# Performance work log

Hardware: AMD Instinct MI355X
Metric: run time of the kernel (lower is better)

Reference implementation:

```python
import jax, jax.numpy as jnp
import numpy as np

IN_CHANNELS = 3
WINDOW_SIZE = 11
SIGMA = 1.5
PAD = WINDOW_SIZE // 2


def _create_window():
    # NOTE: faithful to the original repo, the exponent is POSITIVE (a known
    # bug in AntixK/PyTorch-VAE); we replicate the exact math.
    x = np.arange(WINDOW_SIZE, dtype=np.float64)
    k = np.exp((x - WINDOW_SIZE // 2) ** 2 / (2.0 * SIGMA ** 2))
    k = (k / k.sum()).astype(np.float32)
    w2d = np.outer(k, k)  # [K, K]
    # depthwise kernel, OIHW with groups=C -> [C, 1, K, K]
    return jnp.asarray(np.broadcast_to(w2d, (IN_CHANNELS, 1, WINDOW_SIZE, WINDOW_SIZE)).copy())


def _dwconv(x, w):
    return jax.lax.conv_general_dilated(
        x, w, window_strides=(1, 1), padding=[(PAD, PAD), (PAD, PAD)],
        feature_group_count=IN_CHANNELS,
        dimension_numbers=('NCHW', 'OIHW', 'NCHW'))


def _avg_pool2(x):
    B, C, H, W = x.shape
    return x.reshape(B, C, H // 2, 2, W // 2, 2).mean(axis=(3, 5))


def _ssim(img1, img2, window):
    mu1 = _dwconv(img1, window)
    mu2 = _dwconv(img2, window)
    mu1_sq = mu1 * mu1
    mu2_sq = mu2 * mu2
    mu1_mu2 = mu1 * mu2
    sigma1_sq = _dwconv(img1 * img1, window) - mu1_sq
    sigma2_sq = _dwconv(img2 * img2, window) - mu2_sq
    sigma12 = _dwconv(img1 * img2, window) - mu1_mu2
    C1 = 0.01 ** 2
    C2 = 0.03 ** 2
    v1 = 2.0 * sigma12 + C2
    v2 = sigma1_sq + sigma2_sq + C2
    cs = jnp.mean(v1 / v2)
    ssim_map = (2.0 * mu1_mu2 + C1) * v1 / ((mu1_sq + mu2_sq + C1) * v2)
    return jnp.mean(ssim_map), cs  # size_average=True


def setup_inputs() -> dict:
    key = jax.random.key(0)
    k1, k2 = jax.random.split(key)
    shape = (32, 3, 512, 512)
    img1 = jax.random.uniform(k1, shape, dtype=jnp.float32)
    img2 = jax.random.uniform(k2, shape, dtype=jnp.float32)
    return {"img1": img1, "img2": img2}


def reference(img1, img2):
    weights = jnp.asarray([0.0448, 0.2856, 0.3001, 0.2363, 0.1333], dtype=jnp.float32)
    window = _create_window()
    mssim, mcs = [], []
    for _ in range(5):
        sim, cs = _ssim(img1, img2, window)
        mssim.append(sim)
        mcs.append(cs)
        img1 = _avg_pool2(img1)
        img2 = _avg_pool2(img2)
    mssim = jnp.stack(mssim)
    mcs = jnp.stack(mcs)
    pow1 = mcs ** weights
    pow2 = mssim ** weights
    output = jnp.prod(pow1[:-1] * pow2[-1])
    return 1.0 - output
```

## Files before the change

### kernel.cpp

```cpp
#include <hip/hip_runtime.h>
#include <cmath>

typedef short bf16x8 __attribute__((ext_vector_type(8)));
typedef float f32x4 __attribute__((ext_vector_type(4)));

struct Coeffs { float k[11]; };

__device__ __forceinline__ ushort f2bf(float f) {
    unsigned u = __float_as_uint(f);
    u += 0x7fff + ((u >> 16) & 1);
    return (ushort)(u >> 16);
}

__device__ __forceinline__ unsigned pk2(float lo, float hi) {
    unsigned d;
    asm("v_cvt_pk_bf16_f32 %0, %1, %2" : "=v"(d) : "v"(lo), "v"(hi));
    return d;
}

__device__ __forceinline__ float frcp(float x) { return __builtin_amdgcn_rcpf(x); }

__device__ __forceinline__ float4 ld4s(const float* __restrict__ p, int r, int c, int H, int W) {
    float4 v = make_float4(0.f, 0.f, 0.f, 0.f);
    if (r >= 0 && r < H) {
        const float* row = p + (size_t)r * W;
        if (c >= 0 && c + 3 < W) {
            v = *reinterpret_cast<const float4*>(row + c);
        } else {
            if (c + 0 >= 0 && c + 0 < W) v.x = row[c + 0];
            if (c + 1 >= 0 && c + 1 < W) v.y = row[c + 1];
            if (c + 2 >= 0 && c + 2 < W) v.z = row[c + 2];
            if (c + 3 >= 0 && c + 3 < W) v.w = row[c + 3];
        }
    }
    return v;
}

union FragU { ushort us[8]; bf16x8 v; uint4 q; };
union RdU   { uint4 q; bf16x8 v; };

__global__ __launch_bounds__(64)
void init_frag_kernel(uint4* __restrict__ tab, Coeffs cf) {
    const int lane = threadIdx.x;
    const int lj   = lane & 15;
    const int part = lane >> 4;
    FragU bHf, aVf;
    #pragma unroll
    for (int i = 0; i < 8; ++i) {
        const int kk = part * 8 + i;
        const int tH = kk - lj - 3;
        const int tV = kk - lj;
        float vH = 0.f, vV = 0.f;
        #pragma unroll
        for (int tt = 0; tt < 11; ++tt) {
            vH = (tH == tt) ? cf.k[tt] : vH;
            vV = (tV == tt) ? cf.k[tt] : vV;
        }
        bHf.us[i] = f2bf(vH);
        aVf.us[i] = f2bf(vV);
    }
    tab[lane]      = bHf.q;
    tab[64 + lane] = aVf.q;
}

__global__ __launch_bounds__(256)
void ssim_level_mfma(const float* __restrict__ i1, const float* __restrict__ i2,
                     float* __restrict__ o1, float* __restrict__ o2,
                     int H, int W,
                     double* __restrict__ accum,
                     const uint4* __restrict__ frag_tab)
{
    __shared__ __align__(16) ushort H_T[5][32][64];
    __shared__ double red[2][4];

    const int tid  = threadIdx.x;
    const int lane = tid & 63;
    const int lj   = lane & 15;
    const int part = lane >> 4;
    const int swz  = (lane & 7) << 4;
    const int wv   = __builtin_amdgcn_readfirstlane(tid) >> 6;

    const int bc = blockIdx.z;
    const int r0 = blockIdx.y * 32;
    const int c0 = blockIdx.x * 32;
    const float* p1 = i1 + (size_t)bc * H * W;
    const float* p2 = i2 + (size_t)bc * H * W;

    RdU bHu, aVu;
    bHu.q = frag_tab[lane];
    aVu.q = frag_tab[64 + lane];
    const bf16x8 bH = bHu.v;
    const bf16x8 aV = aVu.v;

    const f32x4 zf = {0.f, 0.f, 0.f, 0.f};

    if (wv < 3) {
        const int gr = r0 - 5 + wv * 16 + lj;
        char* st = (char*)&H_T[0][0][0] + lj * 128 + ((wv * 32 + part * 8) ^ swz);
        #pragma unroll
        for (int cg = 0; cg < 2; ++cg) {
            const int gc = c0 - 8 + cg * 16 + part * 8;
            float a8[8], b8[8];
            if (gr >= 0 && gr < H && gc >= 0 && gc + 8 <= W) {
                const size_t idx = (size_t)gr * W + gc;
                float4 va0 = *reinterpret_cast<const float4*>(p1 + idx);
                float4 va1 = *reinterpret_cast<const float4*>(p1 + idx + 4);
                float4 vb0 = *reinterpret_cast<const float4*>(p2 + idx);
                float4 vb1 = *reinterpret_cast<const float4*>(p2 + idx + 4);
                a8[0]=va0.x; a8[1]=va0.y; a8[2]=va0.z; a8[3]=va0.w;
                a8[4]=va1.x; a8[5]=va1.y; a8[6]=va1.z; a8[7]=va1.w;
                b8[0]=vb0.x; b8[1]=vb0.y; b8[2]=vb0.z; b8[3]=vb0.w;
                b8[4]=vb1.x; b8[5]=vb1.y; b8[6]=vb1.z; b8[7]=vb1.w;
            } else {
                float4 va0 = ld4s(p1, gr, gc, H, W);
                float4 va1 = ld4s(p1, gr, gc + 4, H, W);
                float4 vb0 = ld4s(p2, gr, gc, H, W);
                float4 vb1 = ld4s(p2, gr, gc + 4, H, W);
                a8[0]=va0.x; a8[1]=va0.y; a8[2]=va0.z; a8[3]=va0.w;
                a8[4]=va1.x; a8[5]=va1.y; a8[6]=va1.z; a8[7]=va1.w;
                b8[0]=vb0.x; b8[1]=vb0.y; b8[2]=vb0.z; b8[3]=vb0.w;
                b8[4]=vb1.x; b8[5]=vb1.y; b8[6]=vb1.z; b8[7]=vb1.w;
            }

            unsigned pkf[5][4];
            #pragma unroll
            for (int e = 0; e < 4; ++e) {
                const float a0 = a8[2*e], a1 = a8[2*e+1];
                const float b0 = b8[2*e], b1 = b8[2*e+1];
                pkf[0][e] = pk2(a0, a1);
                pkf[1][e] = pk2(b0, b1);
                pkf[2][e] = pk2(a0*a0, a1*a1);
                pkf[3][e] = pk2(b0*b0, b1*b1);
                pkf[4][e] = pk2(a0*b0, a1*b1);
            }
            #pragma unroll
            for (int s = 0; s < 5; ++s) {
                RdU fr;
                fr.q.x = pkf[s][0]; fr.q.y = pkf[s][1];
                fr.q.z = pkf[s][2]; fr.q.w = pkf[s][3];
                f32x4 d = __builtin_amdgcn_mfma_f32_16x16x32_bf16(fr.v, bH, zf, 0, 0, 0);
                *(uint2*)(st + cg * 2048 + s * 4096)
                    = make_uint2(pk2(d[0], d[1]), pk2(d[2], d[3]));
            }
        }
    } else if (o1 != nullptr) {
        const int p = tid - 192;
        const int i = p & 15;
        const int h = p >> 4;
        const size_t idx = (size_t)(r0 + 2 * i) * W + (c0 + 8 * h);
        const float* pa = p1 + idx;
        const float* pb = p2 + idx;
        float4 a00 = *reinterpret_cast<const float4*>(pa);
        float4 a01 = *reinterpret_cast<const float4*>(pa + 4);
        float4 a10 = *reinterpret_cast<const float4*>(pa + W);
        float4 a11 = *reinterpret_cast<const float4*>(pa + W + 4);
        float4 b00 = *reinterpret_cast<const float4*>(pb);
        float4 b01 = *reinterpret_cast<const float4*>(pb + 4);
        float4 b10 = *reinterpret_cast<const float4*>(pb + W);
        float4 b11 = *reinterpret_cast<const float4*>(pb + W + 4);
        float4 oa, ob;
        oa.x = 0.25f*(a00.x+a00.y+a10.x+a10.y); oa.y = 0.25f*(a00.z+a00.w+a10.z+a10.w);
        oa.z = 0.25f*(a01.x+a01.y+a11.x+a11.y); oa.w = 0.25f*(a01.z+a01.w+a11.z+a11.w);
        ob.x = 0.25f*(b00.x+b00.y+b10.x+b10.y); ob.y = 0.25f*(b00.z+b00.w+b10.z+b10.w);
        ob.z = 0.25f*(b01.x+b01.y+b11.x+b11.y); ob.w = 0.25f*(b01.z+b01.w+b11.z+b11.w);
        const int W2 = W >> 1;
        const size_t base = (size_t)bc * (size_t)(H >> 1) * W2
                          + (size_t)(r0/2 + i) * W2 + (c0/2 + 4*h);
        *reinterpret_cast<float4*>(o1 + base) = oa;
        *reinterpret_cast<float4*>(o2 + base) = ob;
    }
    __syncthreads();

    const int rg2 = wv >> 1;
    const int cg2 = wv & 1;
    const char* hb = (const char*)&H_T[0][0][0] + cg2 * 2048 + lj * 128
                   + ((rg2 * 32 + part * 16) ^ swz);
    f32x4 acc[5];
    #pragma unroll
    for (int s = 0; s < 5; ++s) {
        RdU br;
        br.q = *(const uint4*)(hb + s * 4096);
        acc[s] = __builtin_amdgcn_mfma_f32_16x16x32_bf16(aV, br.v, zf, 0, 0, 0);
    }

    const float C1 = 1e-4f, C2 = 9e-4f;
    float ssim_acc = 0.f, cs_acc = 0.f;
    #pragma unroll
    for (int r = 0; r < 4; ++r) {
        const float mu1 = acc[0][r], mu2 = acc[1][r];
        const float m11 = acc[2][r], m22 = acc[3][r], m12 = acc[4][r];
        const float mu1s = mu1 * mu1, mu2s = mu2 * mu2, mu12 = mu1 * mu2;
        const float v1 = 2.f * (m12 - mu12) + C2;
        const float v2 = (m11 - mu1s) + (m22 - mu2s) + C2;
        const float r2 = frcp(v2);
        const float rd = frcp(mu1s + mu2s + C1);
        cs_acc   += v1 * r2;
        ssim_acc += (2.f * mu12 + C1) * v1 * r2 * rd;
    }

    #pragma unroll
    for (int off = 32; off > 0; off >>= 1) {
        ssim_acc += __shfl_down(ssim_acc, off);
        cs_acc   += __shfl_down(cs_acc, off);
    }
    if (lane == 0) { red[0][wv] = (double)ssim_acc; red[1][wv] = (double)cs_acc; }
    __syncthreads();
    if (tid == 0) {
        double s = red[0][0] + red[0][1] + red[0][2] + red[0][3];
        double c = red[1][0] + red[1][1] + red[1][2] + red[1][3];
        int slot = (blockIdx.x + blockIdx.y * 3 + blockIdx.z * 7) & 63;
        atomicAdd(&accum[slot], s);
        atomicAdd(&accum[64 + slot], c);
    }
}

#define SPF 33
#define HRF 42

__global__ __launch_bounds__(256)
void ssim_level_f32(const float* __restrict__ i1, const float* __restrict__ i2,
                    float* __restrict__ o1, float* __restrict__ o2,
                    int H, int W,
                    double* __restrict__ accum, Coeffs cf)
{
    __shared__ __align__(16) float varr[5][HRF][SPF];
    __shared__ __align__(16) float phl[2][16][16];
    __shared__ double red[2][4];

    const int tid = threadIdx.x;
    const int bc  = blockIdx.z;
    const int r0 = blockIdx.y * 32;
    const int c0 = blockIdx.x * 32;
    const float* p1 = i1 + (size_t)bc * H * W;
    const float* p2 = i2 + (size_t)bc * H * W;

    const int row_rel = tid >> 2;
    const int j  = tid & 3;
    const int cl = 8 * j;
    float hpA[4], hpB[4];
    bool pool_thread = false;

    if (tid < HRF * 4) {
        const int gr  = r0 + row_rel - 5;
        const int gcb = c0 + cl - 8;

        float a[24], b[24];
        if (gr >= 0 && gr < H && gcb >= 0 && gcb + 24 <= W) {
            const size_t idx = (size_t)gr * W + gcb;
            const float* pa = p1 + idx;
            const float* pb = p2 + idx;
            #pragma unroll
            for (int g = 0; g < 6; ++g) {
                float4 va = *reinterpret_cast<const float4*>(pa + 4 * g);
                float4 vb = *reinterpret_cast<const float4*>(pb + 4 * g);
                a[4*g+0]=va.x; a[4*g+1]=va.y; a[4*g+2]=va.z; a[4*g+3]=va.w;
                b[4*g+0]=vb.x; b[4*g+1]=vb.y; b[4*g+2]=vb.z; b[4*g+3]=vb.w;
            }
        } else {
            #pragma unroll
            for (int g = 0; g < 6; ++g) {
                float4 va = ld4s(p1, gr, gcb + 4 * g, H, W);
                float4 vb = ld4s(p2, gr, gcb + 4 * g, H, W);
                a[4*g+0]=va.x; a[4*g+1]=va.y; a[4*g+2]=va.z; a[4*g+3]=va.w;
                b[4*g+0]=vb.x; b[4*g+1]=vb.y; b[4*g+2]=vb.z; b[4*g+3]=vb.w;
            }
        }

        float acc[5][8] = {};
        #pragma unroll
        for (int i = 0; i < 24; ++i) {
            float av = a[i], bv = b[i];
            float pa2 = av * av, pb2 = bv * bv, pab = av * bv;
            #pragma unroll
            for (int jo = 0; jo < 8; ++jo) {
                const int t = i - 3 - jo;
                if (t >= 0 && t <= 10) {
                    const float kk = cf.k[t];
                    acc[0][jo] += kk * av;  acc[1][jo] += kk * bv;
                    acc[2][jo] += kk * pa2; acc[3][jo] += kk * pb2;
                    acc[4][jo] += kk * pab;
                }
            }
        }
        #pragma unroll
        for (int s = 0; s < 5; ++s) {
            *reinterpret_cast<float4*>(&varr[s][row_rel][cl]) =
                make_float4(acc[s][0], acc[s][1], acc[s][2], acc[s][3]);
            *reinterpret_cast<float4*>(&varr[s][row_rel][cl + 4]) =
                make_float4(acc[s][4], acc[s][5], acc[s][6], acc[s][7]);
        }

        if (o1 != nullptr && row_rel >= 5 && row_rel <= 36) {
            #pragma unroll
            for (int p = 0; p < 4; ++p) {
                hpA[p] = a[8 + 2*p] + a[9 + 2*p];
                hpB[p] = b[8 + 2*p] + b[9 + 2*p];
            }
            if (row_rel & 1) {
                const int i = (row_rel - 5) >> 1;
                *reinterpret_cast<float4*>(&phl[0][i][4*j]) = make_float4(hpA[0],hpA[1],hpA[2],hpA[3]);
                *reinterpret_cast<float4*>(&phl[1][i][4*j]) = make_float4(hpB[0],hpB[1],hpB[2],hpB[3]);
            } else if (row_rel >= 6) {
                pool_thread = true;
            }
        }
    }
    __syncthreads();

    if (pool_thread) {
        const int i = (row_rel - 6) >> 1;
        const int W2 = W >> 1;
        float4 qa = *reinterpret_cast<const float4*>(&phl[0][i][4*j]);
        float4 qb = *reinterpret_cast<const float4*>(&phl[1][i][4*j]);
        qa.x = 0.25f*(qa.x + hpA[0]); qa.y = 0.25f*(qa.y + hpA[1]);
        qa.z = 0.25f*(qa.z + hpA[2]); qa.w = 0.25f*(qa.w + hpA[3]);
        qb.x = 0.25f*(qb.x + hpB[0]); qb.y = 0.25f*(qb.y + hpB[1]);
        qb.z = 0.25f*(qb.z + hpB[2]); qb.w = 0.25f*(qb.w + hpB[3]);
        const size_t base = (size_t)bc * (size_t)(H >> 1) * W2
                          + (size_t)(r0/2 + i) * W2 + (c0/2 + 4*j);
        *reinterpret_cast<float4*>(o1 + base) = qa;
        *reinterpret_cast<float4*>(o2 + base) = qb;
    }

    const int col = tid & 31;
    const int rg  = tid >> 5;

    float acc[5][4] = {};
    #pragma unroll
    for (int t = 0; t < 14; ++t) {
        const int m = rg * 4 + t;
        #pragma unroll
        for (int s = 0; s < 5; ++s) {
            const float val = varr[s][m][col];
            #pragma unroll
            for (int i = 0; i < 4; ++i) {
                const int tap = t - i;
                if (tap >= 0 && tap <= 10) acc[s][i] += cf.k[tap] * val;
            }
        }
    }

    const float C1 = 1e-4f, C2 = 9e-4f;
    float ssim_acc = 0.f, cs_acc = 0.f;
    #pragma unroll
    for (int i = 0; i < 4; ++i) {
        const float mu1 = acc[0][i], mu2 = acc[1][i];
        const float m11 = acc[2][i], m22 = acc[3][i], m12 = acc[4][i];
        const float mu1s = mu1 * mu1, mu2s = mu2 * mu2, mu12 = mu1 * mu2;
        const float v1 = 2.f * (m12 - mu12) + C2;
        const float v2 = (m11 - mu1s) + (m22 - mu2s) + C2;
        const float r2 = frcp(v2);
        const float rd = frcp(mu1s + mu2s + C1);
        cs_acc   += v1 * r2;
        ssim_acc += (2.f * mu12 + C1) * v1 * r2 * rd;
    }

    #pragma unroll
    for (int off = 32; off > 0; off >>= 1) {
        ssim_acc += __shfl_down(ssim_acc, off);
        cs_acc   += __shfl_down(cs_acc, off);
    }
    const int wave = tid >> 6, lane = tid & 63;
    if (lane == 0) { red[0][wave] = (double)ssim_acc; red[1][wave] = (double)cs_acc; }
    __syncthreads();
    if (tid == 0) {
        double s = red[0][0] + red[0][1] + red[0][2] + red[0][3];
        double c = red[1][0] + red[1][1] + red[1][2] + red[1][3];
        int slot = (blockIdx.x + blockIdx.y * 3 + blockIdx.z * 7) & 63;
        atomicAdd(&accum[slot], s);
        atomicAdd(&accum[64 + slot], c);
    }
}

__global__ __launch_bounds__(64)
void finalize_kernel(const double* __restrict__ accum,
                     float* __restrict__ out, int BC)
{
    __shared__ double sums[5][2];
    int tid = threadIdx.x;
    for (int lvl = 0; lvl < 5; ++lvl) {
        for (int m = 0; m < 2; ++m) {
            double v = accum[(lvl * 2 + m) * 64 + tid];
            for (int off = 32; off > 0; off >>= 1) v += __shfl_down(v, off);
            if (tid == 0) sums[lvl][m] = v;
        }
    }
    __syncthreads();
    if (tid == 0) {
        const double w[5] = {0.0448, 0.2856, 0.3001, 0.2363, 0.1333};
        double prod = 1.0;
        for (int lvl = 0; lvl < 5; ++lvl) {
            int hw = (512 >> lvl);
            double cnt = (double)BC * (double)hw * (double)hw;
            double mssim = sums[lvl][0] / cnt;
            double mcs   = sums[lvl][1] / cnt;
            if (lvl < 4) {
                prod *= pow(mcs, w[lvl]);
            } else {
                double p2 = pow(mssim, w[4]);
                prod *= p2 * p2 * p2 * p2;
            }
        }
        out[0] = (float)(1.0 - prod);
    }
}

extern "C" void kernel_launch(void* const* d_in, const int* in_sizes, int n_in,
                              void* d_out, int out_size, void* d_ws, size_t ws_size,
                              hipStream_t stream) {
    const float* img1 = (const float*)d_in[0];
    const float* img2 = (const float*)d_in[1];
    float* out = (float*)d_out;
    char* ws = (char*)d_ws;

    const int BC = in_sizes[0] / (512 * 512);

    double* accum = (double*)ws;
    uint4*  ftab  = (uint4*)(ws + 6144);
    size_t off = 8192;
    float* lvl1[5] = {nullptr, nullptr, nullptr, nullptr, nullptr};
    float* lvl2[5] = {nullptr, nullptr, nullptr, nullptr, nullptr};
    for (int l = 1; l < 5; ++l) {
        size_t hw = (size_t)(512 >> l) * (512 >> l);
        lvl1[l] = (float*)(ws + off); off += (size_t)BC * hw * sizeof(float);
        lvl2[l] = (float*)(ws + off); off += (size_t)BC * hw * sizeof(float);
    }

    hipMemsetAsync(accum, 0, 5 * 2 * 64 * sizeof(double), stream);

    Coeffs cf;
    {
        double kd[11], sum = 0.0;
        for (int i = 0; i < 11; ++i) { kd[i] = exp(((double)((i-5)*(i-5))) / 4.5); sum += kd[i]; }
        for (int i = 0; i < 11; ++i) cf.k[i] = (float)(kd[i] / sum);
    }

    init_frag_kernel<<<1, 64, 0, stream>>>(ftab, cf);

    const float* cur1 = img1;
    const float* cur2 = img2;
    for (int lvl = 0; lvl < 5; ++lvl) {
        int H = 512 >> lvl, W = H;
        dim3 grid(W / 32, H / 32, BC);
        float* n1 = (lvl < 4) ? lvl1[lvl + 1] : nullptr;
        float* n2 = (lvl < 4) ? lvl2[lvl + 1] : nullptr;
        if (lvl < 2) {
            ssim_level_mfma<<<grid, 256, 0, stream>>>(cur1, cur2, n1, n2, H, W,
                                                      accum + lvl * 128, ftab);
        } else {
            ssim_level_f32<<<grid, 256, 0, stream>>>(cur1, cur2, n1, n2, H, W,
                                                     accum + lvl * 128, cf);
        }
        cur1 = n1; cur2 = n2;
    }

    finalize_kernel<<<1, 64, 0, stream>>>(accum, out, BC);
}
```

Baseline: 195.0 us.

## Make MFMA SSIM kernel persistent with register double-buffered tile prefetch

Turns the MFMA level kernel into a persistent grid-stride loop over flattened tiles, with the grid capped at 2048 blocks. Global loads for the next tile go into a second register buffer while the current tile is convolved and reduced, so load latency overlaps compute. The downsample wave now reuses the same prefetched registers. The cost is extra registers per thread, which may lower occupancy, plus a fixed grid size that may balance work unevenly.

```diff
diff --git a/kernel.cpp b/kernel.cpp
--- a/kernel.cpp
+++ b/kernel.cpp
@@ -63,70 +63,77 @@
     tab[64 + lane] = aVf.q;
 }
 
-__global__ __launch_bounds__(256)
-void ssim_level_mfma(const float* __restrict__ i1, const float* __restrict__ i2,
-                     float* __restrict__ o1, float* __restrict__ o2,
-                     int H, int W,
-                     double* __restrict__ accum,
-                     const uint4* __restrict__ frag_tab)
+__device__ __forceinline__ void issue_tile_loads(
+    const float* __restrict__ i1, const float* __restrict__ i2,
+    int H, int W, int bc, int r0, int c0,
+    int wv, int lj, int part,
+    float (&SA)[2][8], float (&SB)[2][8])
 {
-    __shared__ __align__(16) ushort H_T[5][32][64];
-    __shared__ double red[2][4];
-
-    const int tid  = threadIdx.x;
-    const int lane = tid & 63;
-    const int lj   = lane & 15;
-    const int part = lane >> 4;
-    const int swz  = (lane & 7) << 4;
-    const int wv   = __builtin_amdgcn_readfirstlane(tid) >> 6;
-
-    const int bc = blockIdx.z;
-    const int r0 = blockIdx.y * 32;
-    const int c0 = blockIdx.x * 32;
     const float* p1 = i1 + (size_t)bc * H * W;
     const float* p2 = i2 + (size_t)bc * H * W;
-
-    RdU bHu, aVu;
-    bHu.q = frag_tab[lane];
-    aVu.q = frag_tab[64 + lane];
-    const bf16x8 bH = bHu.v;
-    const bf16x8 aV = aVu.v;
-
-    const f32x4 zf = {0.f, 0.f, 0.f, 0.f};
-
     if (wv < 3) {
         const int gr = r0 - 5 + wv * 16 + lj;
-        char* st = (char*)&H_T[0][0][0] + lj * 128 + ((wv * 32 + part * 8) ^ swz);
         #pragma unroll
         for (int cg = 0; cg < 2; ++cg) {
             const int gc = c0 - 8 + cg * 16 + part * 8;
-            float a8[8], b8[8];
+            float4 va0, va1, vb0, vb1;
             if (gr >= 0 && gr < H && gc >= 0 && gc + 8 <= W) {
                 const size_t idx = (size_t)gr * W + gc;
-                float4 va0 = *reinterpret_cast<const float4*>(p1 + idx);
-                float4 va1 = *reinterpret_cast<const float4*>(p1 + idx + 4);
-                float4 vb0 = *reinterpret_cast<const float4*>(p2 + idx);
-                float4 vb1 = *reinterpret_cast<const float4*>(p2 + idx + 4);
-                a8[0]=va0.x; a8[1]=va0.y; a8[2]=va0.z; a8[3]=va0.w;
-                a8[4]=va1.x; a8[5]=va1.y; a8[6]=va1.z; a8[7]=va1.w;
-                b8[0]=vb0.x; b8[1]=vb0.y; b8[2]=vb0.z; b8[3]=vb0.w;
-                b8[4]=vb1.x; b8[5]=vb1.y; b8[6]=vb1.z; b8[7]=vb1.w;
+                va0 = *reinterpret_cast<const float4*>(p1 + idx);
+                va1 = *reinterpret_cast<const float4*>(p1 + idx + 4);
+                vb0 = *reinterpret_cast<const float4*>(p2 + idx);
+                vb1 = *reinterpret_cast<const float4*>(p2 + idx + 4);
             } else {
-                float4 va0 = ld4s(p1, gr, gc, H, W);
-                float4 va1 = ld4s(p1, gr, gc + 4, H, W);
-                float4 vb0 = ld4s(p2, gr, gc, H, W);
-                float4 vb1 = ld4s(p2, gr, gc + 4, H, W);
-                a8[0]=va0.x; a8[1]=va0.y; a8[2]=va0.z; a8[3]=va0.w;
-                a8[4]=va1.x; a8[5]=va1.y; a8[6]=va1.z; a8[7]=va1.w;
-                b8[0]=vb0.x; b8[1]=vb0.y; b8[2]=vb0.z; b8[3]=vb0.w;
-                b8[4]=vb1.x; b8[5]=vb1.y; b8[6]=vb1.z; b8[7]=vb1.w;
-            }
-
+                va0 = ld4s(p1, gr, gc, H, W);
+                va1 = ld4s(p1, gr, gc + 4, H, W);
+                vb0 = ld4s(p2, gr, gc, H, W);
+                vb1 = ld4s(p2, gr, gc + 4, H, W);
+            }
+            SA[cg][0]=va0.x; SA[cg][1]=va0.y; SA[cg][2]=va0.z; SA[cg][3]=va0.w;
+            SA[cg][4]=va1.x; SA[cg][5]=va1.y; SA[cg][6]=va1.z; SA[cg][7]=va1.w;
+            SB[cg][0]=vb0.x; SB[cg][1]=vb0.y; SB[cg][2]=vb0.z; SB[cg][3]=vb0.w;
+            SB[cg][4]=vb1.x; SB[cg][5]=vb1.y; SB[cg][6]=vb1.z; SB[cg][7]=vb1.w;
+        }
+    } else {
+        const size_t idx = (size_t)(r0 + 2 * lj) * W + (c0 + part * 8);
+        float4 va0 = *reinterpret_cast<const float4*>(p1 + idx);
+        float4 va1 = *reinterpret_cast<const float4*>(p1 + idx + 4);
+        float4 va2 = *reinterpret_cast<const float4*>(p1 + idx + W);
+        float4 va3 = *reinterpret_cast<const float4*>(p1 + idx + W + 4);
+        float4 vb0 = *reinterpret_cast<const float4*>(p2 + idx);
+        float4 vb1 = *reinterpret_cast<const float4*>(p2 + idx + 4);
+        float4 vb2 = *reinterpret_cast<const float4*>(p2 + idx + W);
+        float4 vb3 = *reinterpret_cast<const float4*>(p2 + idx + W + 4);
+        SA[0][0]=va0.x; SA[0][1]=va0.y; SA[0][2]=va0.z; SA[0][3]=va0.w;
+        SA[0][4]=va1.x; SA[0][5]=va1.y; SA[0][6]=va1.z; SA[0][7]=va1.w;
+        SA[1][0]=va2.x; SA[1][1]=va2.y; SA[1][2]=va2.z; SA[1][3]=va2.w;
+        SA[1][4]=va3.x; SA[1][5]=va3.y; SA[1][6]=va3.z; SA[1][7]=va3.w;
+        SB[0][0]=vb0.x; SB[0][1]=vb0.y; SB[0][2]=vb0.z; SB[0][3]=vb0.w;
+        SB[0][4]=vb1.x; SB[0][5]=vb1.y; SB[0][6]=vb1.z; SB[0][7]=vb1.w;
+        SB[1][0]=vb2.x; SB[1][1]=vb2.y; SB[1][2]=vb2.z; SB[1][3]=vb2.w;
+        SB[1][4]=vb3.x; SB[1][5]=vb3.y; SB[1][6]=vb3.z; SB[1][7]=vb3.w;
+    }
+}
+
+__device__ __forceinline__ void compute_tile(
+    ushort* H_T0, double (*red)[4],
+    const bf16x8 bH, const bf16x8 aV,
+    char* st, const char* hb,
+    int wv, int lane, int tid, int lj, int part,
+    int H, int W, int bc, int r0, int c0, int tile_idx,
+    float (&SA)[2][8], float (&SB)[2][8],
+    float* __restrict__ o1, float* __restrict__ o2,
+    double* __restrict__ accum)
+{
+    const f32x4 zf = {0.f, 0.f, 0.f, 0.f};
+    if (wv < 3) {
+        #pragma unroll
+        for (int cg = 0; cg < 2; ++cg) {
             unsigned pkf[5][4];
             #pragma unroll
             for (int e = 0; e < 4; ++e) {
-                const float a0 = a8[2*e], a1 = a8[2*e+1];
-                const float b0 = b8[2*e], b1 = b8[2*e+1];
+                const float a0 = SA[cg][2*e], a1 = SA[cg][2*e+1];
+                const float b0 = SB[cg][2*e], b1 = SB[cg][2*e+1];
                 pkf[0][e] = pk2(a0, a1);
                 pkf[1][e] = pk2(b0, b1);
                 pkf[2][e] = pk2(a0*a0, a1*a1);
@@ -143,38 +150,24 @@
                     = make_uint2(pk2(d[0], d[1]), pk2(d[2], d[3]));
             }
         }
-    } else if (o1 != nullptr) {
-        const int p = tid - 192;
-        const int i = p & 15;
-        const int h = p >> 4;
-        const size_t idx = (size_t)(r0 + 2 * i) * W + (c0 + 8 * h);
-        const float* pa = p1 + idx;
-        const float* pb = p2 + idx;
-        float4 a00 = *reinterpret_cast<const float4*>(pa);
-        float4 a01 = *reinterpret_cast<const float4*>(pa + 4);
-        float4 a10 = *reinterpret_cast<const float4*>(pa + W);
-        float4 a11 = *reinterpret_cast<const float4*>(pa + W + 4);
-        float4 b00 = *reinterpret_cast<const float4*>(pb);
-        float4 b01 = *reinterpret_cast<const float4*>(pb + 4);
-        float4 b10 = *reinterpret_cast<const float4*>(pb + W);
-        float4 b11 = *reinterpret_cast<const float4*>(pb + W + 4);
+    } else {
         float4 oa, ob;
-        oa.x = 0.25f*(a00.x+a00.y+a10.x+a10.y); oa.y = 0.25f*(a00.z+a00.w+a10.z+a10.w);
-        oa.z = 0.25f*(a01.x+a01.y+a11.x+a11.y); oa.w = 0.25f*(a01.z+a01.w+a11.z+a11.w);
-        ob.x = 0.25f*(b00.x+b00.y+b10.x+b10.y); ob.y = 0.25f*(b00.z+b00.w+b10.z+b10.w);
-        ob.z = 0.25f*(b01.x+b01.y+b11.x+b11.y); ob.w = 0.25f*(b01.z+b01.w+b11.z+b11.w);
+        oa.x = 0.25f*(SA[0][0]+SA[0][1]+SA[1][0]+SA[1][1]);
+        oa.y = 0.25f*(SA[0][2]+SA[0][3]+SA[1][2]+SA[1][3]);
+        oa.z = 0.25f*(SA[0][4]+SA[0][5]+SA[1][4]+SA[1][5]);
+        oa.w = 0.25f*(SA[0][6]+SA[0][7]+SA[1][6]+SA[1][7]);
+        ob.x = 0.25f*(SB[0][0]+SB[0][1]+SB[1][0]+SB[1][1]);
+        ob.y = 0.25f*(SB[0][2]+SB[0][3]+SB[1][2]+SB[1][3]);
+        ob.z = 0.25f*(SB[0][4]+SB[0][5]+SB[1][4]+SB[1][5]);
+        ob.w = 0.25f*(SB[0][6]+SB[0][7]+SB[1][6]+SB[1][7]);
         const int W2 = W >> 1;
         const size_t base = (size_t)bc * (size_t)(H >> 1) * W2
-                          + (size_t)(r0/2 + i) * W2 + (c0/2 + 4*h);
+                          + (size_t)(r0 / 2 + lj) * W2 + (c0 / 2 + part * 4);
         *reinterpret_cast<float4*>(o1 + base) = oa;
         *reinterpret_cast<float4*>(o2 + base) = ob;
     }
     __syncthreads();
 
-    const int rg2 = wv >> 1;
-    const int cg2 = wv & 1;
-    const char* hb = (const char*)&H_T[0][0][0] + cg2 * 2048 + lj * 128
-                   + ((rg2 * 32 + part * 16) ^ swz);
     f32x4 acc[5];
     #pragma unroll
     for (int s = 0; s < 5; ++s) {
@@ -208,9 +201,79 @@
     if (tid == 0) {
         double s = red[0][0] + red[0][1] + red[0][2] + red[0][3];
         double c = red[1][0] + red[1][1] + red[1][2] + red[1][3];
-        int slot = (blockIdx.x + blockIdx.y * 3 + blockIdx.z * 7) & 63;
+        int slot = tile_idx & 63;
         atomicAdd(&accum[slot], s);
         atomicAdd(&accum[64 + slot], c);
+    }
+}
+
+__global__ __launch_bounds__(256)
+void ssim_level_mfma(const float* __restrict__ i1, const float* __restrict__ i2,
+                     float* __restrict__ o1, float* __restrict__ o2,
+                     int H, int W, int logT, int ntiles,
+                     double* __restrict__ accum,
+                     const uint4* __restrict__ frag_tab)
+{
+    __shared__ __align__(16) ushort H_T[5][32][64];
+    __shared__ double red[2][4];
+
+    const int tid  = threadIdx.x;
+    const int lane = tid & 63;
+    const int lj   = lane & 15;
+    const int part = lane >> 4;
+    const int swz  = (lane & 7) << 4;
+    const int wv   = __builtin_amdgcn_readfirstlane(tid) >> 6;
+
+    RdU bHu, aVu;
+    bHu.q = frag_tab[lane];
+    aVu.q = frag_tab[64 + lane];
+    const bf16x8 bH = bHu.v;
+    const bf16x8 aV = aVu.v;
+
+    char* st = (char*)&H_T[0][0][0] + lj * 128 + (((wv < 3 ? wv : 0) * 32 + part * 8) ^ swz);
+    const int rg2 = wv >> 1, cg2 = wv & 1;
+    const char* hb = (const char*)&H_T[0][0][0] + cg2 * 2048 + lj * 128
+                   + ((rg2 * 32 + part * 16) ^ swz);
+
+    const int tmask  = (1 << logT) - 1;
+    const int stride = gridDim.x;
+
+    int idx = blockIdx.x;
+    if (idx >= ntiles) return;
+    int bc = idx >> (2 * logT);
+    int r0 = ((idx >> logT) & tmask) * 32;
+    int c0 = (idx & tmask) * 32;
+
+    float S0A[2][8], S0B[2][8], S1A[2][8], S1B[2][8];
+    issue_tile_loads(i1, i2, H, W, bc, r0, c0, wv, lj, part, S0A, S0B);
+
+    int nbc = 0, nr0 = 0, nc0 = 0;
+    while (true) {
+        int nidx = idx + stride;
+        bool has = nidx < ntiles;
+        if (has) {
+            nbc = nidx >> (2 * logT);
+            nr0 = ((nidx >> logT) & tmask) * 32;
+            nc0 = (nidx & tmask) * 32;
+            issue_tile_loads(i1, i2, H, W, nbc, nr0, nc0, wv, lj, part, S1A, S1B);
+        }
+        compute_tile(&H_T[0][0][0], red, bH, aV, st, hb, wv, lane, tid, lj, part,
+                     H, W, bc, r0, c0, idx, S0A, S0B, o1, o2, accum);
+        if (!has) break;
+        idx = nidx; bc = nbc; r0 = nr0; c0 = nc0;
+
+        nidx = idx + stride;
+        has = nidx < ntiles;
+        if (has) {
+            nbc = nidx >> (2 * logT);
+            nr0 = ((nidx >> logT) & tmask) * 32;
+            nc0 = (nidx & tmask) * 32;
+            issue_tile_loads(i1, i2, H, W, nbc, nr0, nc0, wv, lj, part, S0A, S0B);
+        }
+        compute_tile(&H_T[0][0][0], red, bH, aV, st, hb, wv, lane, tid, lj, part,
+                     H, W, bc, r0, c0, idx, S1A, S1B, o1, o2, accum);
+        if (!has) break;
+        idx = nidx; bc = nbc; r0 = nr0; c0 = nc0;
     }
 }
 
@@ -441,13 +504,18 @@
     const float* cur2 = img2;
     for (int lvl = 0; lvl < 5; ++lvl) {
         int H = 512 >> lvl, W = H;
-        dim3 grid(W / 32, H / 32, BC);
         float* n1 = (lvl < 4) ? lvl1[lvl + 1] : nullptr;
         float* n2 = (lvl < 4) ? lvl2[lvl + 1] : nullptr;
         if (lvl < 2) {
+            int T = W / 32;
+            int logT = (lvl == 0) ? 4 : 3;
+            int ntiles = T * T * BC;
+            int grid = ntiles < 2048 ? ntiles : 2048;
             ssim_level_mfma<<<grid, 256, 0, stream>>>(cur1, cur2, n1, n2, H, W,
+                                                      logT, ntiles,
                                                       accum + lvl * 128, ftab);
         } else {
+            dim3 grid(W / 32, H / 32, BC);
             ssim_level_f32<<<grid, 256, 0, stream>>>(cur1, cur2, n1, n2, H, W,
                                                      accum + lvl * 128, cf);
         }
```

Result: slower. 225.0 us (+15.4%).

## Stage raw input tile in shared memory with cooperative coalesced loads

Applied to the files above, without the earlier changes.

All 256 threads now cooperatively load the 48x48 input halo tile for both images into a shared-memory buffer before any compute. The horizontal MFMA pass and the 2x2 average-pool writer then read from shared memory instead of issuing their own global loads. This removes duplicate global reads between the pooling wave and the conv waves and spreads the loads over all four waves. The cost is an extra barrier, about 20 KB more LDS per block (which may lower occupancy), and possible bank conflicts from the 52-float row pitch.

```diff
diff --git a/kernel.cpp b/kernel.cpp
--- a/kernel.cpp
+++ b/kernel.cpp
@@ -5,6 +5,8 @@
 typedef float f32x4 __attribute__((ext_vector_type(4)));
 
 struct Coeffs { float k[11]; };
+
+#define RPITCH 52
 
 __device__ __forceinline__ ushort f2bf(float f) {
     unsigned u = __float_as_uint(f);
@@ -70,6 +72,7 @@
                      double* __restrict__ accum,
                      const uint4* __restrict__ frag_tab)
 {
+    __shared__ __align__(16) float  RAW[2][48][RPITCH];
     __shared__ __align__(16) ushort H_T[5][32][64];
     __shared__ double red[2][4];
 
@@ -92,35 +95,45 @@
     const bf16x8 bH = bHu.v;
     const bf16x8 aV = aVu.v;
 
+    {
+        const bool interior = (r0 >= 5) && (r0 + 43 <= H) && (c0 >= 8) && (c0 + 40 <= W);
+        #pragma unroll
+        for (int img = 0; img < 2; ++img) {
+            const float* p = img ? p2 : p1;
+            #pragma unroll
+            for (int it = 0; it < 3; ++it) {
+                const int idx = tid + it * 256;
+                if (idx < 576) {
+                    const int row  = idx / 12;
+                    const int colg = idx - row * 12;
+                    const int gr = r0 - 5 + row;
+                    const int gc = c0 - 8 + 4 * colg;
+                    float4 v;
+                    if (interior) {
+                        v = *reinterpret_cast<const float4*>(p + (size_t)gr * W + gc);
+                    } else {
+                        v = ld4s(p, gr, gc, H, W);
+                    }
+                    *reinterpret_cast<float4*>(&RAW[img][row][4 * colg]) = v;
+                }
+            }
+        }
+    }
+    __syncthreads();
+
     const f32x4 zf = {0.f, 0.f, 0.f, 0.f};
-
     if (wv < 3) {
-        const int gr = r0 - 5 + wv * 16 + lj;
+        const int row = wv * 16 + lj;
         char* st = (char*)&H_T[0][0][0] + lj * 128 + ((wv * 32 + part * 8) ^ swz);
         #pragma unroll
         for (int cg = 0; cg < 2; ++cg) {
-            const int gc = c0 - 8 + cg * 16 + part * 8;
-            float a8[8], b8[8];
-            if (gr >= 0 && gr < H && gc >= 0 && gc + 8 <= W) {
-                const size_t idx = (size_t)gr * W + gc;
-                float4 va0 = *reinterpret_cast<const float4*>(p1 + idx);
-                float4 va1 = *reinterpret_cast<const float4*>(p1 + idx + 4);
-                float4 vb0 = *reinterpret_cast<const float4*>(p2 + idx);
-                float4 vb1 = *reinterpret_cast<const float4*>(p2 + idx + 4);
-                a8[0]=va0.x; a8[1]=va0.y; a8[2]=va0.z; a8[3]=va0.w;
-                a8[4]=va1.x; a8[5]=va1.y; a8[6]=va1.z; a8[7]=va1.w;
-                b8[0]=vb0.x; b8[1]=vb0.y; b8[2]=vb0.z; b8[3]=vb0.w;
-                b8[4]=vb1.x; b8[5]=vb1.y; b8[6]=vb1.z; b8[7]=vb1.w;
-            } else {
-                float4 va0 = ld4s(p1, gr, gc, H, W);
-                float4 va1 = ld4s(p1, gr, gc + 4, H, W);
-                float4 vb0 = ld4s(p2, gr, gc, H, W);
-                float4 vb1 = ld4s(p2, gr, gc + 4, H, W);
-                a8[0]=va0.x; a8[1]=va0.y; a8[2]=va0.z; a8[3]=va0.w;
-                a8[4]=va1.x; a8[5]=va1.y; a8[6]=va1.z; a8[7]=va1.w;
-                b8[0]=vb0.x; b8[1]=vb0.y; b8[2]=vb0.z; b8[3]=vb0.w;
-                b8[4]=vb1.x; b8[5]=vb1.y; b8[6]=vb1.z; b8[7]=vb1.w;
-            }
+            const int cb = cg * 16 + part * 8;
+            float4 va0 = *reinterpret_cast<const float4*>(&RAW[0][row][cb]);
+            float4 va1 = *reinterpret_cast<const float4*>(&RAW[0][row][cb + 4]);
+            float4 vb0 = *reinterpret_cast<const float4*>(&RAW[1][row][cb]);
+            float4 vb1 = *reinterpret_cast<const float4*>(&RAW[1][row][cb + 4]);
+            float a8[8] = {va0.x, va0.y, va0.z, va0.w, va1.x, va1.y, va1.z, va1.w};
+            float b8[8] = {vb0.x, vb0.y, vb0.z, vb0.w, vb1.x, vb1.y, vb1.z, vb1.w};
 
             unsigned pkf[5][4];
             #pragma unroll
@@ -144,35 +157,30 @@
             }
         }
     } else if (o1 != nullptr) {
-        const int p = tid - 192;
-        const int i = p & 15;
-        const int h = p >> 4;
-        const size_t idx = (size_t)(r0 + 2 * i) * W + (c0 + 8 * h);
-        const float* pa = p1 + idx;
-        const float* pb = p2 + idx;
-        float4 a00 = *reinterpret_cast<const float4*>(pa);
-        float4 a01 = *reinterpret_cast<const float4*>(pa + 4);
-        float4 a10 = *reinterpret_cast<const float4*>(pa + W);
-        float4 a11 = *reinterpret_cast<const float4*>(pa + W + 4);
-        float4 b00 = *reinterpret_cast<const float4*>(pb);
-        float4 b01 = *reinterpret_cast<const float4*>(pb + 4);
-        float4 b10 = *reinterpret_cast<const float4*>(pb + W);
-        float4 b11 = *reinterpret_cast<const float4*>(pb + W + 4);
+        const int ra = 5 + 2 * lj;
+        const int cb = 8 + 8 * part;
+        float4 a0 = *reinterpret_cast<const float4*>(&RAW[0][ra][cb]);
+        float4 a1 = *reinterpret_cast<const float4*>(&RAW[0][ra][cb + 4]);
+        float4 a2 = *reinterpret_cast<const float4*>(&RAW[0][ra + 1][cb]);
+        float4 a3 = *reinterpret_cast<const float4*>(&RAW[0][ra + 1][cb + 4]);
+        float4 b0 = *reinterpret_cast<const float4*>(&RAW[1][ra][cb]);
+        float4 b1 = *reinterpret_cast<const float4*>(&RAW[1][ra][cb + 4]);
+        float4 b2 = *reinterpret_cast<const float4*>(&RAW[1][ra + 1][cb]);
+        float4 b3 = *reinterpret_cast<const float4*>(&RAW[1][ra + 1][cb + 4]);
         float4 oa, ob;
-        oa.x = 0.25f*(a00.x+a00.y+a10.x+a10.y); oa.y = 0.25f*(a00.z+a00.w+a10.z+a10.w);
-        oa.z = 0.25f*(a01.x+a01.y+a11.x+a11.y); oa.w = 0.25f*(a01.z+a01.w+a11.z+a11.w);
-        ob.x = 0.25f*(b00.x+b00.y+b10.x+b10.y); ob.y = 0.25f*(b00.z+b00.w+b10.z+b10.w);
-        ob.z = 0.25f*(b01.x+b01.y+b11.x+b11.y); ob.w = 0.25f*(b01.z+b01.w+b11.z+b11.w);
+        oa.x = 0.25f*(a0.x+a0.y+a2.x+a2.y); oa.y = 0.25f*(a0.z+a0.w+a2.z+a2.w);
+        oa.z = 0.25f*(a1.x+a1.y+a3.x+a3.y); oa.w = 0.25f*(a1.z+a1.w+a3.z+a3.w);
+        ob.x = 0.25f*(b0.x+b0.y+b2.x+b2.y); ob.y = 0.25f*(b0.z+b0.w+b2.z+b2.w);
+        ob.z = 0.25f*(b1.x+b1.y+b3.x+b3.y); ob.w = 0.25f*(b1.z+b1.w+b3.z+b3.w);
         const int W2 = W >> 1;
         const size_t base = (size_t)bc * (size_t)(H >> 1) * W2
-                          + (size_t)(r0/2 + i) * W2 + (c0/2 + 4*h);
+                          + (size_t)(r0 / 2 + lj) * W2 + (c0 / 2 + part * 4);
         *reinterpret_cast<float4*>(o1 + base) = oa;
         *reinterpret_cast<float4*>(o2 + base) = ob;
     }
     __syncthreads();
 
-    const int rg2 = wv >> 1;
-    const int cg2 = wv & 1;
+    const int rg2 = wv >> 1, cg2 = wv & 1;
     const char* hb = (const char*)&H_T[0][0][0] + cg2 * 2048 + lj * 128
                    + ((rg2 * 32 + part * 16) ^ swz);
     f32x4 acc[5];
```

Result: slower. 217.6 us (+11.6%).
